# Performance work log

Hardware: AMD Instinct MI355X
Metric: run time of the kernel (lower is better)

The kernel has to match this reference:

```python
import jax, jax.numpy as jnp
import numpy as np

D_ORIG, D_HEAD, N_HEAD = 64, 32, 8
D_EMB = D_HEAD * N_HEAD


def setup_inputs() -> dict:
    key = jax.random.key(0)
    ks = jax.random.split(key, 9)
    b, l = 1, 512
    x = jax.random.normal(ks[0], (b, l, D_ORIG), dtype=jnp.float32)
    e = jax.random.normal(ks[1], (b, l, l, D_ORIG), dtype=jnp.float32)
    s = 1.0 / np.sqrt(D_ORIG)
    Wq = jax.random.uniform(ks[2], (D_ORIG, D_EMB), jnp.float32, -s, s)
    Wk = jax.random.uniform(ks[3], (D_ORIG, D_EMB), jnp.float32, -s, s)
    Wv = jax.random.uniform(ks[4], (D_ORIG, D_EMB), jnp.float32, -s, s)
    We = jax.random.uniform(ks[5], (D_ORIG, D_EMB), jnp.float32, -s, s)
    so = 1.0 / np.sqrt(D_EMB)
    Wo = jax.random.uniform(ks[6], (D_EMB, D_ORIG), jnp.float32, -so, so)
    bo = jax.random.uniform(ks[7], (D_ORIG,), jnp.float32, -so, so)
    return {"x": x, "e": e, "Wq": Wq, "Wk": Wk, "Wv": Wv, "We": We, "Wo": Wo, "bo": bo}


def reference(x, e, Wq, Wk, Wv, We, Wo, bo):
    b, l, _ = x.shape
    # projections
    q = (x @ Wq).reshape(b, l, N_HEAD, D_HEAD).transpose(0, 2, 1, 3)  # b n l d
    k = (x @ Wk).reshape(b, l, N_HEAD, D_HEAD).transpose(0, 2, 1, 3)
    v = (x @ Wv).reshape(b, l, N_HEAD, D_HEAD).transpose(0, 2, 1, 3)
    ee = (e @ We).reshape(b, l, l, N_HEAD, D_HEAD).transpose(0, 3, 1, 2, 4)  # b n i j d
    # edge-biased keys/values: broadcast add over query index i
    kb = k[:, :, None, :, :] + ee  # b n i j d
    logit = jnp.einsum('bnid,bnijd->bnij', q, kb) * (D_HEAD ** -0.5)
    attn = jax.nn.softmax(logit, axis=-1)
    vb = v[:, :, None, :, :] + ee  # b n i j d
    out = jnp.einsum('bnij,bnijd->bnid', attn, vb)  # b n i d
    out = out.transpose(0, 2, 1, 3).reshape(b, l, D_EMB)
    return out @ Wo + bo
```

## Files before the change

kernel.cpp:

```cpp
#include <hip/hip_runtime.h>

#define SCALE 0.17677669529663687f
#define PSTR 513

__global__ __launch_bounds__(512, 4) void fused_kernel(
    const float* __restrict__ e, const float* __restrict__ x,
    const float* __restrict__ Wq, const float* __restrict__ Wk,
    const float* __restrict__ We, const float* __restrict__ Wv,
    const float* __restrict__ Wo, const float* __restrict__ bo,
    float* __restrict__ out) {
  const int t = threadIdx.x, i = blockIdx.x;
  __shared__ float s_x[64];
  __shared__ __align__(16) float s_q[256];
  __shared__ __align__(16) float s_qc[1024];
  __shared__ __align__(16) float s_p[8 * PSTR];
  __shared__ __align__(16) float s_pt[512 * 8];
  __shared__ __align__(16) float s_part[8 * 1024];
  __shared__ float s_ae[512], s_px[512];
  __shared__ float s_emb[256];
  __shared__ float s_op[8 * 64];

  if (t < 64) s_x[t] = x[i * 64 + t];
  __syncthreads();
  if (t < 256) {
    float a = 0;
#pragma unroll 8
    for (int c = 0; c < 64; ++c) a += s_x[c] * Wq[c * 256 + t];
    s_q[t] = a * SCALE;
  }
  __syncthreads();
  {
    const int c = t >> 3, h = t & 7;
    const float4* wer = (const float4*)(We + c * 256 + h * 32);
    const float4* wkr = (const float4*)(Wk + c * 256 + h * 32);
    const float4* qr = (const float4*)(s_q + h * 32);
    float se = 0, sk = 0;
#pragma unroll
    for (int u = 0; u < 8; ++u) {
      float4 w1 = wer[u], w2 = wkr[u], qv = qr[u];
      se += qv.x * w1.x + qv.y * w1.y + qv.z * w1.z + qv.w * w1.w;
      sk += qv.x * w2.x + qv.y * w2.y + qv.z * w2.z + qv.w * w2.w;
    }
    s_qc[c * 16 + h] = se;
    s_qc[c * 16 + 8 + h] = sk;
  }
  __syncthreads();

  {
    const int j = t;
    const float4* erow = (const float4*)(e + (size_t)(i * 512 + j) * 64);
    const float4* xrow = (const float4*)(x + j * 64);
    float acc[8];
#pragma unroll
    for (int h = 0; h < 8; ++h) acc[h] = 0.f;
#pragma unroll 4
    for (int c4 = 0; c4 < 16; ++c4) {
      float4 E = erow[c4];
      float4 X = xrow[c4];
      const float* qc = s_qc + c4 * 64;
#pragma unroll
      for (int h = 0; h < 8; ++h) {
        acc[h] += E.x * qc[h]      + E.y * qc[16 + h]
                + E.z * qc[32 + h] + E.w * qc[48 + h]
                + X.x * qc[8 + h]  + X.y * qc[24 + h]
                + X.z * qc[40 + h] + X.w * qc[56 + h];
      }
    }
#pragma unroll
    for (int h = 0; h < 8; ++h) s_p[h * PSTR + j] = acc[h];
  }
  __syncthreads();

  {
    const int n = t >> 6, l64 = t & 63;
    float m = -1e30f;
#pragma unroll
    for (int u = 0; u < 8; ++u) m = fmaxf(m, s_p[n * PSTR + l64 + u * 64]);
#pragma unroll
    for (int off = 32; off; off >>= 1) m = fmaxf(m, __shfl_xor(m, off, 64));
    float pv[8];
    float sum = 0;
#pragma unroll
    for (int u = 0; u < 8; ++u) {
      pv[u] = __expf(s_p[n * PSTR + l64 + u * 64] - m);
      sum += pv[u];
    }
#pragma unroll
    for (int off = 32; off; off >>= 1) sum += __shfl_xor(sum, off, 64);
    const float inv = 1.0f / sum;
#pragma unroll
    for (int u = 0; u < 8; ++u) s_pt[(l64 + u * 64) * 8 + n] = pv[u] * inv;
  }
  __syncthreads();

  {
    const int lane = t & 63, w = t >> 6;
    float ae[8], px[8];
#pragma unroll
    for (int h = 0; h < 8; ++h) { ae[h] = 0.f; px[h] = 0.f; }
    const float* ep = e + (size_t)i * 32768 + (size_t)w * 4096 + lane;
    const float* xp = x + w * 4096 + lane;
#pragma unroll 4
    for (int jj = 0; jj < 64; ++jj) {
      const int j = w * 64 + jj;
      float ev = ep[jj * 64];
      float xv = xp[jj * 64];
      const float4* pt = (const float4*)(s_pt + j * 8);
      float4 p0 = pt[0], p1 = pt[1];
      ae[0] += p0.x * ev; ae[1] += p0.y * ev; ae[2] += p0.z * ev; ae[3] += p0.w * ev;
      ae[4] += p1.x * ev; ae[5] += p1.y * ev; ae[6] += p1.z * ev; ae[7] += p1.w * ev;
      px[0] += p0.x * xv; px[1] += p0.y * xv; px[2] += p0.z * xv; px[3] += p0.w * xv;
      px[4] += p1.x * xv; px[5] += p1.y * xv; px[6] += p1.z * xv; px[7] += p1.w * xv;
    }
#pragma unroll
    for (int h = 0; h < 8; ++h) {
      s_part[w * 1024 + h * 64 + lane] = ae[h];
      s_part[w * 1024 + 512 + h * 64 + lane] = px[h];
    }
  }
  __syncthreads();

  {
    float va = 0, vp = 0;
#pragma unroll
    for (int w = 0; w < 8; ++w) {
      va += s_part[w * 1024 + t];
      vp += s_part[w * 1024 + 512 + t];
    }
    s_ae[t] = va; s_px[t] = vp;
  }
  __syncthreads();

  {
    const int nd = t & 255, ch = t >> 8, hn = nd >> 5;
    float emb = 0;
    const int cb = ch * 32;
#pragma unroll 8
    for (int c = cb; c < cb + 32; ++c)
      emb += s_ae[hn * 64 + c] * We[c * 256 + nd] + s_px[hn * 64 + c] * Wv[c * 256 + nd];
    s_part[ch * 256 + nd] = emb;
  }
  __syncthreads();
  if (t < 256) s_emb[t] = s_part[t] + s_part[256 + t];
  __syncthreads();
  {
    const int o = t & 63, mc = t >> 6;
    float oo = 0;
#pragma unroll 8
    for (int m2 = mc * 32; m2 < mc * 32 + 32; ++m2) oo += s_emb[m2] * Wo[m2 * 64 + o];
    s_op[mc * 64 + o] = oo;
  }
  __syncthreads();
  if (t < 64) {
    float r = bo[t];
#pragma unroll
    for (int w = 0; w < 8; ++w) r += s_op[w * 64 + t];
    out[i * 64 + t] = r;
  }
}

extern "C" void kernel_launch(void* const* d_in, const int* in_sizes, int n_in,
                              void* d_out, int out_size, void* d_ws, size_t ws_size,
                              hipStream_t stream) {
  const float* x  = (const float*)d_in[0];
  const float* e  = (const float*)d_in[1];
  const float* Wq = (const float*)d_in[2];
  const float* Wk = (const float*)d_in[3];
  const float* Wv = (const float*)d_in[4];
  const float* We = (const float*)d_in[5];
  const float* Wo = (const float*)d_in[6];
  const float* bo = (const float*)d_in[7];
  float* out = (float*)d_out;

  hipLaunchKernelGGL(fused_kernel, dim3(512), dim3(512), 0, stream,
                     e, x, Wq, Wk, We, Wv, Wo, bo, out);
}
```

Measured before the change: 139.5 us.

## Double block to 1024 threads with register-resident softmax and atomic reductions

```diff
diff --git a/kernel.cpp b/kernel.cpp
--- a/kernel.cpp
+++ b/kernel.cpp
@@ -1,25 +1,29 @@
 #include <hip/hip_runtime.h>
 
 #define SCALE 0.17677669529663687f
-#define PSTR 513
 
-__global__ __launch_bounds__(512, 4) void fused_kernel(
+__global__ __launch_bounds__(1024, 8) void fused_kernel(
     const float* __restrict__ e, const float* __restrict__ x,
     const float* __restrict__ Wq, const float* __restrict__ Wk,
     const float* __restrict__ We, const float* __restrict__ Wv,
     const float* __restrict__ Wo, const float* __restrict__ bo,
     float* __restrict__ out) {
   const int t = threadIdx.x, i = blockIdx.x;
+  const int lane = t & 63, w = t >> 6;
+  const int j = t & 511;
+  const int hb = (t >> 9) * 4;
+
   __shared__ float s_x[64];
   __shared__ __align__(16) float s_q[256];
   __shared__ __align__(16) float s_qc[1024];
-  __shared__ __align__(16) float s_p[8 * PSTR];
-  __shared__ __align__(16) float s_pt[512 * 8];
-  __shared__ __align__(16) float s_part[8 * 1024];
-  __shared__ float s_ae[512], s_px[512];
-  __shared__ float s_emb[256];
-  __shared__ float s_op[8 * 64];
+  __shared__ __align__(16) float s_pt[4096];
+  __shared__ __align__(16) float s_red[64];
+  __shared__ __align__(16) float s_red2[64];
+  __shared__ float s_inv[8];
+  __shared__ __align__(16) float s_ae[512];
+  __shared__ __align__(16) float s_px[512];
 
+  if (t < 512) { s_ae[t] = 0.f; s_px[t] = 0.f; }
   if (t < 64) s_x[t] = x[i * 64 + t];
   __syncthreads();
   if (t < 256) {
@@ -30,82 +34,92 @@
   }
   __syncthreads();
   {
-    const int c = t >> 3, h = t & 7;
-    const float4* wer = (const float4*)(We + c * 256 + h * 32);
-    const float4* wkr = (const float4*)(Wk + c * 256 + h * 32);
+    const int c = t >> 4, hv = t & 15, which = hv >> 3, h = hv & 7;
+    const float* W = which ? Wk : We;
+    const float4* wr = (const float4*)(W + c * 256 + h * 32);
     const float4* qr = (const float4*)(s_q + h * 32);
-    float se = 0, sk = 0;
+    float s = 0;
 #pragma unroll
     for (int u = 0; u < 8; ++u) {
-      float4 w1 = wer[u], w2 = wkr[u], qv = qr[u];
-      se += qv.x * w1.x + qv.y * w1.y + qv.z * w1.z + qv.w * w1.w;
-      sk += qv.x * w2.x + qv.y * w2.y + qv.z * w2.z + qv.w * w2.w;
+      float4 wv4 = wr[u], qv = qr[u];
+      s += qv.x * wv4.x + qv.y * wv4.y + qv.z * wv4.z + qv.w * wv4.w;
     }
-    s_qc[c * 16 + h] = se;
-    s_qc[c * 16 + 8 + h] = sk;
+    s_qc[c * 16 + which * 8 + h] = s;
   }
   __syncthreads();
 
+  float acc[4];
   {
-    const int j = t;
     const float4* erow = (const float4*)(e + (size_t)(i * 512 + j) * 64);
     const float4* xrow = (const float4*)(x + j * 64);
-    float acc[8];
-#pragma unroll
-    for (int h = 0; h < 8; ++h) acc[h] = 0.f;
+    acc[0] = acc[1] = acc[2] = acc[3] = 0.f;
 #pragma unroll 4
     for (int c4 = 0; c4 < 16; ++c4) {
       float4 E = erow[c4];
       float4 X = xrow[c4];
-      const float* qc = s_qc + c4 * 64;
+      const float* qc = s_qc + c4 * 64 + hb;
 #pragma unroll
-      for (int h = 0; h < 8; ++h) {
-        acc[h] += E.x * qc[h]      + E.y * qc[16 + h]
-                + E.z * qc[32 + h] + E.w * qc[48 + h]
-                + X.x * qc[8 + h]  + X.y * qc[24 + h]
-                + X.z * qc[40 + h] + X.w * qc[56 + h];
+      for (int hh = 0; hh < 4; ++hh) {
+        acc[hh] += E.x * qc[hh]      + E.y * qc[16 + hh]
+                 + E.z * qc[32 + hh] + E.w * qc[48 + hh]
+                 + X.x * qc[8 + hh]  + X.y * qc[24 + hh]
+                 + X.z * qc[40 + hh] + X.w * qc[56 + hh];
       }
     }
+  }
+
+  {
 #pragma unroll
-    for (int h = 0; h < 8; ++h) s_p[h * PSTR + j] = acc[h];
+    for (int hh = 0; hh < 4; ++hh) {
+      float m = acc[hh];
+#pragma unroll
+      for (int off = 32; off; off >>= 1) m = fmaxf(m, __shfl_xor(m, off, 64));
+      if (lane == 0) s_red[w * 4 + hh] = m;
+    }
   }
   __syncthreads();
+  {
+    const int half8 = (t >> 9) * 8;
+    float4 M = ((const float4*)s_red)[half8];
+#pragma unroll
+    for (int ww = 1; ww < 8; ++ww) {
+      float4 a = ((const float4*)s_red)[half8 + ww];
+      M.x = fmaxf(M.x, a.x); M.y = fmaxf(M.y, a.y);
+      M.z = fmaxf(M.z, a.z); M.w = fmaxf(M.w, a.w);
+    }
+    acc[0] = __expf(acc[0] - M.x);
+    acc[1] = __expf(acc[1] - M.y);
+    acc[2] = __expf(acc[2] - M.z);
+    acc[3] = __expf(acc[3] - M.w);
+    *(float4*)(s_pt + j * 8 + hb) = make_float4(acc[0], acc[1], acc[2], acc[3]);
+#pragma unroll
+    for (int hh = 0; hh < 4; ++hh) {
+      float s = acc[hh];
+#pragma unroll
+      for (int off = 32; off; off >>= 1) s += __shfl_xor(s, off, 64);
+      if (lane == 0) s_red2[w * 4 + hh] = s;
+    }
+  }
+  __syncthreads();
+  if (t < 8) {
+    const int half32 = (t >> 2) * 32, hh = t & 3;
+    float s = 0;
+#pragma unroll
+    for (int ww = 0; ww < 8; ++ww) s += s_red2[half32 + ww * 4 + hh];
+    s_inv[t] = 1.0f / s;
+  }
 
   {
-    const int n = t >> 6, l64 = t & 63;
-    float m = -1e30f;
-#pragma unroll
-    for (int u = 0; u < 8; ++u) m = fmaxf(m, s_p[n * PSTR + l64 + u * 64]);
-#pragma unroll
-    for (int off = 32; off; off >>= 1) m = fmaxf(m, __shfl_xor(m, off, 64));
-    float pv[8];
-    float sum = 0;
-#pragma unroll
-    for (int u = 0; u < 8; ++u) {
-      pv[u] = __expf(s_p[n * PSTR + l64 + u * 64] - m);
-      sum += pv[u];
-    }
-#pragma unroll
-    for (int off = 32; off; off >>= 1) sum += __shfl_xor(sum, off, 64);
-    const float inv = 1.0f / sum;
-#pragma unroll
-    for (int u = 0; u < 8; ++u) s_pt[(l64 + u * 64) * 8 + n] = pv[u] * inv;
-  }
-  __syncthreads();
-
-  {
-    const int lane = t & 63, w = t >> 6;
     float ae[8], px[8];
 #pragma unroll
     for (int h = 0; h < 8; ++h) { ae[h] = 0.f; px[h] = 0.f; }
-    const float* ep = e + (size_t)i * 32768 + (size_t)w * 4096 + lane;
-    const float* xp = x + w * 4096 + lane;
+    const float* ep = e + (size_t)i * 32768 + w * 2048 + lane;
+    const float* xp = x + w * 2048 + lane;
 #pragma unroll 4
-    for (int jj = 0; jj < 64; ++jj) {
-      const int j = w * 64 + jj;
+    for (int jj = 0; jj < 32; ++jj) {
       float ev = ep[jj * 64];
       float xv = xp[jj * 64];
-      const float4* pt = (const float4*)(s_pt + j * 8);
+      const float4* pt = (const float4*)(s_pt + (w * 32 + jj) * 8);
       float4 p0 = pt[0], p1 = pt[1];
       ae[0] += p0.x * ev; ae[1] += p0.y * ev; ae[2] += p0.z * ev; ae[3] += p0.w * ev;
       ae[4] += p1.x * ev; ae[5] += p1.y * ev; ae[6] += p1.z * ev; ae[7] += p1.w * ev;
@@ -114,47 +128,47 @@
     }
 #pragma unroll
     for (int h = 0; h < 8; ++h) {
-      s_part[w * 1024 + h * 64 + lane] = ae[h];
-      s_part[w * 1024 + 512 + h * 64 + lane] = px[h];
+      atomicAdd(&s_ae[h * 64 + lane], ae[h]);
+      atomicAdd(&s_px[h * 64 + lane], px[h]);
     }
   }
   __syncthreads();
 
-  {
-    float va = 0, vp = 0;
-#pragma unroll
-    for (int w = 0; w < 8; ++w) {
-      va += s_part[w * 1024 + t];
-      vp += s_part[w * 1024 + 512 + t];
-    }
-    s_ae[t] = va; s_px[t] = vp;
+  if (t < 512) {
+    s_ae[t] *= s_inv[t >> 6];
+  } else {
+    const int t2 = t - 512;
+    s_px[t2] *= s_inv[t2 >> 6];
   }
   __syncthreads();
 
+  float* s_eb  = s_pt;
+  float* s_emb = s_pt + 1024;
+  float* s_op  = s_pt + 1280;
   {
     const int nd = t & 255, ch = t >> 8, hn = nd >> 5;
     float emb = 0;
-    const int cb = ch * 32;
-#pragma unroll 8
-    for (int c = cb; c < cb + 32; ++c)
+    const int cb = ch * 16;
+#pragma unroll
+    for (int c = cb; c < cb + 16; ++c)
       emb += s_ae[hn * 64 + c] * We[c * 256 + nd] + s_px[hn * 64 + c] * Wv[c * 256 + nd];
-    s_part[ch * 256 + nd] = emb;
+    s_eb[ch * 256 + nd] = emb;
   }
   __syncthreads();
-  if (t < 256) s_emb[t] = s_part[t] + s_part[256 + t];
+  if (t < 256) s_emb[t] = s_eb[t] + s_eb[256 + t] + s_eb[512 + t] + s_eb[768 + t];
   __syncthreads();
   {
     const int o = t & 63, mc = t >> 6;
     float oo = 0;
-#pragma unroll 8
-    for (int m2 = mc * 32; m2 < mc * 32 + 32; ++m2) oo += s_emb[m2] * Wo[m2 * 64 + o];
+#pragma unroll
+    for (int m2 = mc * 16; m2 < mc * 16 + 16; ++m2) oo += s_emb[m2] * Wo[m2 * 64 + o];
     s_op[mc * 64 + o] = oo;
   }
   __syncthreads();
   if (t < 64) {
     float r = bo[t];
 #pragma unroll
-    for (int w = 0; w < 8; ++w) r += s_op[w * 64 + t];
+    for (int w2 = 0; w2 < 16; ++w2) r += s_op[w2 * 64 + t];
     out[i * 64 + t] = r;
   }
 }
@@ -172,6 +186,6 @@
   const float* bo = (const float*)d_in[7];
   float* out = (float*)d_out;
 
-  hipLaunchKernelGGL(fused_kernel, dim3(512), dim3(512), 0, stream,
+  hipLaunchKernelGGL(fused_kernel, dim3(512), dim3(1024), 0, stream,
                      e, x, Wq, Wk, We, Wv, Wo, bo, out);
 }
```

Measured after the change: 202.7 us. 1.45x slower.

## Shrink shared memory via buffer reuse and LDS atomics to raise occupancy

Applied to the files above, without the earlier changes.

```diff
diff --git a/kernel.cpp b/kernel.cpp
--- a/kernel.cpp
+++ b/kernel.cpp
@@ -3,7 +3,7 @@
 #define SCALE 0.17677669529663687f
 #define PSTR 513
 
-__global__ __launch_bounds__(512, 4) void fused_kernel(
+__global__ __launch_bounds__(512, 8) void fused_kernel(
     const float* __restrict__ e, const float* __restrict__ x,
     const float* __restrict__ Wq, const float* __restrict__ Wk,
     const float* __restrict__ We, const float* __restrict__ Wv,
@@ -14,12 +14,10 @@
   __shared__ __align__(16) float s_q[256];
   __shared__ __align__(16) float s_qc[1024];
   __shared__ __align__(16) float s_p[8 * PSTR];
-  __shared__ __align__(16) float s_pt[512 * 8];
-  __shared__ __align__(16) float s_part[8 * 1024];
-  __shared__ float s_ae[512], s_px[512];
-  __shared__ float s_emb[256];
-  __shared__ float s_op[8 * 64];
+  __shared__ __align__(16) float s_ae[512];
+  __shared__ __align__(16) float s_px[512];
 
+  s_ae[t] = 0.f; s_px[t] = 0.f;
   if (t < 64) s_x[t] = x[i * 64 + t];
   __syncthreads();
   if (t < 256) {
@@ -53,18 +51,20 @@
     float acc[8];
 #pragma unroll
     for (int h = 0; h < 8; ++h) acc[h] = 0.f;
-#pragma unroll 4
+#pragma unroll 2
     for (int c4 = 0; c4 < 16; ++c4) {
       float4 E = erow[c4];
       float4 X = xrow[c4];
-      const float* qc = s_qc + c4 * 64;
-#pragma unroll
-      for (int h = 0; h < 8; ++h) {
-        acc[h] += E.x * qc[h]      + E.y * qc[16 + h]
-                + E.z * qc[32 + h] + E.w * qc[48 + h]
-                + X.x * qc[8 + h]  + X.y * qc[24 + h]
-                + X.z * qc[40 + h] + X.w * qc[56 + h];
-      }
+      const float4* qcv = (const float4*)(s_qc + c4 * 64);
+#define CH(Ec, Xc, B)                                                   \
+  { float4 ce0 = qcv[B], ce1 = qcv[(B) + 1];                            \
+    float4 cx0 = qcv[(B) + 2], cx1 = qcv[(B) + 3];                      \
+    acc[0] += Ec * ce0.x + Xc * cx0.x; acc[1] += Ec * ce0.y + Xc * cx0.y; \
+    acc[2] += Ec * ce0.z + Xc * cx0.z; acc[3] += Ec * ce0.w + Xc * cx0.w; \
+    acc[4] += Ec * ce1.x + Xc * cx1.x; acc[5] += Ec * ce1.y + Xc * cx1.y; \
+    acc[6] += Ec * ce1.z + Xc * cx1.z; acc[7] += Ec * ce1.w + Xc * cx1.w; }
+      CH(E.x, X.x, 0) CH(E.y, X.y, 4) CH(E.z, X.z, 8) CH(E.w, X.w, 12)
+#undef CH
     }
 #pragma unroll
     for (int h = 0; h < 8; ++h) s_p[h * PSTR + j] = acc[h];
@@ -73,23 +73,27 @@
 
   {
     const int n = t >> 6, l64 = t & 63;
+    float lv[8];
     float m = -1e30f;
 #pragma unroll
-    for (int u = 0; u < 8; ++u) m = fmaxf(m, s_p[n * PSTR + l64 + u * 64]);
+    for (int u = 0; u < 8; ++u) {
+      lv[u] = s_p[n * PSTR + l64 + u * 64];
+      m = fmaxf(m, lv[u]);
+    }
 #pragma unroll
     for (int off = 32; off; off >>= 1) m = fmaxf(m, __shfl_xor(m, off, 64));
-    float pv[8];
     float sum = 0;
 #pragma unroll
     for (int u = 0; u < 8; ++u) {
-      pv[u] = __expf(s_p[n * PSTR + l64 + u * 64] - m);
-      sum += pv[u];
+      lv[u] = __expf(lv[u] - m);
+      sum += lv[u];
     }
 #pragma unroll
     for (int off = 32; off; off >>= 1) sum += __shfl_xor(sum, off, 64);
     const float inv = 1.0f / sum;
+    __syncthreads();
 #pragma unroll
-    for (int u = 0; u < 8; ++u) s_pt[(l64 + u * 64) * 8 + n] = pv[u] * inv;
+    for (int u = 0; u < 8; ++u) s_p[(l64 + u * 64) * 8 + n] = lv[u] * inv;
   }
   __syncthreads();
 
@@ -105,7 +109,7 @@
       const int j = w * 64 + jj;
       float ev = ep[jj * 64];
       float xv = xp[jj * 64];
-      const float4* pt = (const float4*)(s_pt + j * 8);
+      const float4* pt = (const float4*)(s_p + j * 8);
       float4 p0 = pt[0], p1 = pt[1];
       ae[0] += p0.x * ev; ae[1] += p0.y * ev; ae[2] += p0.z * ev; ae[3] += p0.w * ev;
       ae[4] += p1.x * ev; ae[5] += p1.y * ev; ae[6] += p1.z * ev; ae[7] += p1.w * ev;
@@ -114,23 +118,15 @@
     }
 #pragma unroll
     for (int h = 0; h < 8; ++h) {
-      s_part[w * 1024 + h * 64 + lane] = ae[h];
-      s_part[w * 1024 + 512 + h * 64 + lane] = px[h];
+      atomicAdd(&s_ae[h * 64 + lane], ae[h]);
+      atomicAdd(&s_px[h * 64 + lane], px[h]);
     }
   }
   __syncthreads();
 
-  {
-    float va = 0, vp = 0;
-#pragma unroll
-    for (int w = 0; w < 8; ++w) {
-      va += s_part[w * 1024 + t];
-      vp += s_part[w * 1024 + 512 + t];
-    }
-    s_ae[t] = va; s_px[t] = vp;
-  }
-  __syncthreads();
-
+  float* s_eb  = s_p;
+  float* s_emb = s_p + 512;
+  float* s_op  = s_p + 1024;
   {
     const int nd = t & 255, ch = t >> 8, hn = nd >> 5;
     float emb = 0;
@@ -138,10 +134,10 @@
 #pragma unroll 8
     for (int c = cb; c < cb + 32; ++c)
       emb += s_ae[hn * 64 + c] * We[c * 256 + nd] + s_px[hn * 64 + c] * Wv[c * 256 + nd];
-    s_part[ch * 256 + nd] = emb;
+    s_eb[ch * 256 + nd] = emb;
   }
   __syncthreads();
-  if (t < 256) s_emb[t] = s_part[t] + s_part[256 + t];
+  if (t < 256) s_emb[t] = s_eb[t] + s_eb[256 + t];
   __syncthreads();
   {
     const int o = t & 63, mc = t >> 6;
@@ -154,7 +150,7 @@
   if (t < 64) {
     float r = bo[t];
 #pragma unroll
-    for (int w = 0; w < 8; ++w) r += s_op[w * 64 + t];
+    for (int w2 = 0; w2 < 8; ++w2) r += s_op[w2 * 64 + t];
     out[i * 64 + t] = r;
   }
 }
```

New measurement: 297.0 us. +112.9%, slower.
